# Kernel optimization log

Measured on AMD Instinct MI355X. Metric: run time of the kernel, lower is better.

The kernel has to match this reference:

```python
import jax, jax.numpy as jnp
import numpy as np

B, C, H, W = 4, 1, 384, 384


def _edt1d_sq(f):
    """Exact 1D squared Euclidean distance transform along last axis.
    f: [..., n] squared-distance field; returns min_j f[..., j] + (i-j)^2.
    Vectorized min-plus convolution with quadratic kernel.
    """
    n = f.shape[-1]
    idx = jnp.arange(n, dtype=f.dtype)
    d2 = (idx[:, None] - idx[None, :]) ** 2  # [n, n]
    # [..., n, n] cost matrix, reduced immediately
    return jnp.min(f[..., None, :] + d2, axis=-1)


def setup_inputs() -> dict:
    key = jax.random.key(0)
    mask = jax.random.randint(key, (B, C, H, W), 0, 2).astype(jnp.float32)
    return {"mask": mask}


def reference(mask) -> jnp.ndarray:
    # ConvertToLuminance: for 4D input with C != 3 path -> channel mean (C=1 -> identity)
    lum = jnp.mean(mask, axis=1, keepdims=True)  # [B,1,H,W]
    # scale to 0..255 if values are in [0,1] (matches `if x.max() <= 1: x *= 255`)
    scaled = jnp.where(jnp.max(lum) <= 1.0, lum * 255.0, lum)
    # cv2.distanceTransform: distance of each nonzero pixel to nearest zero pixel
    fg = scaled > 0.5  # nonzero after uint8 cast (binary 0/255 input)
    h, w = mask.shape[-2], mask.shape[-1]
    LARGE = jnp.asarray(2.0 * (h * h + w * w), dtype=scaled.dtype)
    f = jnp.where(fg, LARGE, jnp.asarray(0.0, scaled.dtype))
    # Separable exact squared EDT (Felzenszwalb-style, brute-force min-plus):
    f = _edt1d_sq(f)  # along W
    f = jnp.swapaxes(_edt1d_sq(jnp.swapaxes(f, -1, -2)), -1, -2)  # along H
    return jnp.sqrt(f)  # [B,1,H,W], orig_dim==4 so shape preserved
```

## Files before the change

### kernel.cpp

```cpp
#include <hip/hip_runtime.h>
#include <hip/hip_bf16.h>


#define HH 384
#define WW 384
#define NB 4
#define WPR 6
#define NPIX (NB * HH * WW)
#define NWORDS (NB * HH * WPR)
#define LARGE_F 589824.0f
#define NOZERO_DIST 768

typedef unsigned long long u64;


__global__ __launch_bounds__(256) void pack_zbits(const float* __restrict__ mask,
                                                  u64* __restrict__ zbits) {
    int idx = blockIdx.x * 256 + threadIdx.x;
    bool isz = mask[idx] < 0.5f;
    u64 w = __ballot(isz);
    if ((threadIdx.x & 63) == 0) zbits[idx >> 6] = w;
}

__device__ __forceinline__ int rowdist(const u64* __restrict__ zr, int x) {
    const int w = x >> 6, xin = x & 63;
    const u64 cur = zr[w];
    int dr = NOZERO_DIST, dl = NOZERO_DIST;
    u64 t = cur >> xin;
    if (t) {
        dr = __ffsll((long long)t) - 1;
    } else {
        for (int ww = w + 1; ww < WPR; ++ww) {
            u64 v = zr[ww];
            if (v) { dr = (ww << 6) + __ffsll((long long)v) - 1 - x; break; }
        }
    }
    u64 u = cur << (63 - xin);
    if (u) {
        dl = __clzll((long long)u);
    } else {
        for (int ww = w - 1; ww >= 0; --ww) {
            u64 v = zr[ww];
            if (v) { dl = x - ((ww << 6) + 63 - __clzll((long long)v)); break; }
        }
    }
    return min(dl, dr);
}

__global__ __launch_bounds__(256) void edt_solve(const u64* __restrict__ zbits,
                                                 float* __restrict__ out) {
    int idx = blockIdx.x * 256 + threadIdx.x;
    int x = idx % WW;
    int y = (idx / WW) % HH;
    int b = idx / (WW * HH);
    const u64* zi = zbits + b * (HH * WPR);

    int r0 = rowdist(zi + y * WPR, x);
    int best = r0 * r0;
    for (int dy = 1; dy < HH; ++dy) {
        int dd = dy * dy;
        if (dd >= best) break;
        if (y - dy >= 0) {
            int r = rowdist(zi + (y - dy) * WPR, x);
            best = min(best, dd + r * r);
        }
        if (y + dy < HH) {
            int r = rowdist(zi + (y + dy) * WPR, x);
            best = min(best, dd + r * r);
        }
    }
    out[idx] = sqrtf((float)best);
}


__global__ __launch_bounds__(WW) void edt_pass1(const float* __restrict__ mask,
                                                float* __restrict__ g) {
    const int row = blockIdx.x;
    const int x = threadIdx.x;
    __shared__ float f[WW];
    const float* m = mask + (size_t)row * WW;
    f[x] = (m[x] > 0.5f) ? LARGE_F : 0.0f;
    __syncthreads();
    float best = 1.0e30f;
    #pragma unroll 8
    for (int j = 0; j < WW; ++j) {
        float d = (float)(x - j);
        best = fminf(best, fmaf(d, d, f[j]));
    }
    g[(size_t)row * WW + x] = best;
}

__global__ __launch_bounds__(HH) void edt_pass2(float* __restrict__ g) {
    const int b = blockIdx.x / WW;
    const int x = blockIdx.x % WW;
    const int y = threadIdx.x;
    __shared__ float f[HH];
    f[y] = g[((size_t)b * HH + y) * WW + x];
    __syncthreads();
    float best = 1.0e30f;
    #pragma unroll 8
    for (int j = 0; j < HH; ++j) {
        float d = (float)(y - j);
        best = fminf(best, fmaf(d, d, f[j]));
    }
    g[((size_t)b * HH + y) * WW + x] = sqrtf(best);
}

extern "C" void kernel_launch(void* const* d_in, const int* in_sizes, int n_in,
                              void* d_out, int out_size, void* d_ws, size_t ws_size,
                              hipStream_t stream) {
    const float* mask = (const float*)d_in[0];
    float* out = (float*)d_out;

    if (ws_size >= (size_t)NWORDS * sizeof(u64)) {
        u64* zbits = (u64*)d_ws;
        const int nb = NPIX / 256;
        pack_zbits<<<nb, 256, 0, stream>>>(mask, zbits);
        edt_solve<<<nb, 256, 0, stream>>>(zbits, out);
    } else {
        edt_pass1<<<NB * HH, WW, 0, stream>>>(mask, out);
        edt_pass2<<<NB * WW, HH, 0, stream>>>(out);
    }
}
```

Measured before the change: 60.13 us.

## Fuse bit packing and EDT solve into one per-row kernel with LDS bitmask

Replaces the separate pack and solve kernels with a single kernel that processes one image row per block. Each block packs only the neighbouring rows it needs into LDS as zero-bit masks. The radius is bounded by the block-wide maximum row distance, found through a wave reduction. This removes a launch and the global workspace round trip, and moves the bit lookups to shared memory. In exchange, each block re-reads and re-ballots up to 2R mask rows from global memory, which duplicates work across blocks.

```diff
diff --git a/kernel.cpp b/kernel.cpp
--- a/kernel.cpp
+++ b/kernel.cpp
@@ -6,26 +6,14 @@
 #define WW 384
 #define NB 4
 #define WPR 6
-#define NPIX (NB * HH * WW)
-#define NWORDS (NB * HH * WPR)
-#define LARGE_F 589824.0f
-#define NOZERO_DIST 768
+#define NOZERO 768
 
 typedef unsigned long long u64;
 
-
-__global__ __launch_bounds__(256) void pack_zbits(const float* __restrict__ mask,
-                                                  u64* __restrict__ zbits) {
-    int idx = blockIdx.x * 256 + threadIdx.x;
-    bool isz = mask[idx] < 0.5f;
-    u64 w = __ballot(isz);
-    if ((threadIdx.x & 63) == 0) zbits[idx >> 6] = w;
-}
-
-__device__ __forceinline__ int rowdist(const u64* __restrict__ zr, int x) {
+__device__ __forceinline__ int rowdist_lds(const u64* zr, int x) {
     const int w = x >> 6, xin = x & 63;
     const u64 cur = zr[w];
-    int dr = NOZERO_DIST, dl = NOZERO_DIST;
+    int dr = NOZERO, dl = NOZERO;
     u64 t = cur >> xin;
     if (t) {
         dr = __ffsll((long long)t) - 1;
@@ -47,63 +35,59 @@
     return min(dl, dr);
 }
 
-__global__ __launch_bounds__(256) void edt_solve(const u64* __restrict__ zbits,
-                                                 float* __restrict__ out) {
-    int idx = blockIdx.x * 256 + threadIdx.x;
-    int x = idx % WW;
-    int y = (idx / WW) % HH;
-    int b = idx / (WW * HH);
-    const u64* zi = zbits + b * (HH * WPR);
+__global__ __launch_bounds__(WW) void edt_fused(const float* __restrict__ mask,
+                                                float* __restrict__ out) {
+    const int rid = blockIdx.x;
+    const int b = rid / HH;
+    const int y = rid % HH;
+    const int x = threadIdx.x;
+    const int wid = x >> 6;
 
-    int r0 = rowdist(zi + y * WPR, x);
+    __shared__ u64 bits[HH][WPR];
+    __shared__ int smax[WW / 64];
+
+    const float* mb = mask + (size_t)b * HH * WW;
+
+    {
+        u64 w = __ballot(mb[y * WW + x] < 0.5f);
+        if ((x & 63) == 0) bits[y][wid] = w;
+    }
+    __syncthreads();
+
+    int r0 = rowdist_lds(bits[y], x);
     int best = r0 * r0;
-    for (int dy = 1; dy < HH; ++dy) {
+
+    int m = r0;
+    #pragma unroll
+    for (int off = 32; off; off >>= 1) m = max(m, __shfl_xor(m, off));
+    if ((x & 63) == 0) smax[wid] = m;
+    __syncthreads();
+    int R = smax[0];
+    #pragma unroll
+    for (int i = 1; i < WW / 64; ++i) R = max(R, smax[i]);
+    R = min(R, HH - 1);
+
+    const int lo = max(0, y - R), hi = min(HH - 1, y + R);
+    for (int r = lo; r <= hi; ++r) {
+        if (r == y) continue;
+        u64 w = __ballot(mb[r * WW + x] < 0.5f);
+        if ((x & 63) == 0) bits[r][wid] = w;
+    }
+    __syncthreads();
+
+    for (int dy = 1; dy <= R; ++dy) {
         int dd = dy * dy;
         if (dd >= best) break;
         if (y - dy >= 0) {
-            int r = rowdist(zi + (y - dy) * WPR, x);
+            int r = rowdist_lds(bits[y - dy], x);
             best = min(best, dd + r * r);
         }
         if (y + dy < HH) {
-            int r = rowdist(zi + (y + dy) * WPR, x);
+            int r = rowdist_lds(bits[y + dy], x);
             best = min(best, dd + r * r);
         }
     }
-    out[idx] = sqrtf((float)best);
-}
-
-
-__global__ __launch_bounds__(WW) void edt_pass1(const float* __restrict__ mask,
-                                                float* __restrict__ g) {
-    const int row = blockIdx.x;
-    const int x = threadIdx.x;
-    __shared__ float f[WW];
-    const float* m = mask + (size_t)row * WW;
-    f[x] = (m[x] > 0.5f) ? LARGE_F : 0.0f;
-    __syncthreads();
-    float best = 1.0e30f;
-    #pragma unroll 8
-    for (int j = 0; j < WW; ++j) {
-        float d = (float)(x - j);
-        best = fminf(best, fmaf(d, d, f[j]));
-    }
-    g[(size_t)row * WW + x] = best;
-}
-
-__global__ __launch_bounds__(HH) void edt_pass2(float* __restrict__ g) {
-    const int b = blockIdx.x / WW;
-    const int x = blockIdx.x % WW;
-    const int y = threadIdx.x;
-    __shared__ float f[HH];
-    f[y] = g[((size_t)b * HH + y) * WW + x];
-    __syncthreads();
-    float best = 1.0e30f;
-    #pragma unroll 8
-    for (int j = 0; j < HH; ++j) {
-        float d = (float)(y - j);
-        best = fminf(best, fmaf(d, d, f[j]));
-    }
-    g[((size_t)b * HH + y) * WW + x] = sqrtf(best);
+    out[(size_t)rid * WW + x] = sqrtf((float)best);
 }
 
 extern "C" void kernel_launch(void* const* d_in, const int* in_sizes, int n_in,
@@ -111,14 +95,5 @@
                               hipStream_t stream) {
     const float* mask = (const float*)d_in[0];
     float* out = (float*)d_out;
-
-    if (ws_size >= (size_t)NWORDS * sizeof(u64)) {
-        u64* zbits = (u64*)d_ws;
-        const int nb = NPIX / 256;
-        pack_zbits<<<nb, 256, 0, stream>>>(mask, zbits);
-        edt_solve<<<nb, 256, 0, stream>>>(zbits, out);
-    } else {
-        edt_pass1<<<NB * HH, WW, 0, stream>>>(mask, out);
-        edt_pass2<<<NB * WW, HH, 0, stream>>>(out);
-    }
+    edt_fused<<<NB * HH, WW, 0, stream>>>(mask, out);
 }
```

New measurement: 65.52 us. +9.0%, slower.
